# Performance work log

Hardware: AMD Instinct MI355X
Metric: run time of the kernel (lower is better)

## Reference

```python
import jax, jax.numpy as jnp
import numpy as np

BSZ, SL, K, D_IN, D_OUT = 2, 1024, 24, 512, 512
K_U, K_Y = 3, 2
USE_HANKEL_L = False


def get_top_eigh(l, k, use_hankel_L):
    i = np.arange(1, l + 1, dtype=np.float64)
    s = i[:, None] + i[None, :]
    if use_hankel_L:
        Z = ((-1.0) ** (s - 2.0) + 1.0) * 8.0 / ((s + 3.0) * (s - 1.0) * (s + 1.0))
    else:
        Z = 2.0 / (s ** 3 - s)
    sigma, phi = np.linalg.eigh(Z)  # ascending
    return jnp.asarray(sigma[-k:], jnp.float32), jnp.asarray(phi[:, -k:], jnp.float32)


def shift(x, k):
    # causal shift along time axis 1, zero-padded at the front
    if k == 0:
        return x
    return jnp.pad(x, ((0, 0), (k, 0), (0, 0)))[:, : x.shape[1]]


def fft_causal_conv(filters, u):
    # filters: (l, k); u: (b, l, d) -> (b, l, k, d) causal convolution per filter
    l = u.shape[1]
    n = 2 * l
    F = jnp.fft.rfft(filters, n=n, axis=0)  # (n//2+1, k)
    U = jnp.fft.rfft(u, n=n, axis=1)        # (b, n//2+1, d)
    Y = jnp.fft.irfft(U[:, :, None, :] * F[None, :, :, None], n=n, axis=1)
    return Y[:, :l].astype(u.dtype)


def compute_ar_u(M_u, u):
    # ar_u[b,t,o] = sum_{i<k_u} M_u[i] @ u_{t-i}
    U = jnp.stack([shift(u, i) for i in range(M_u.shape[0])])  # (k_u, b, l, d_in)
    return jnp.einsum('koi,kbli->blo', M_u, U)


def compute_spectral(u, sigma, phi, M_phi_plus, M_phi_minus, m_y):
    l = u.shape[1]
    phi_s = phi * sigma ** 0.25  # eigenvalue-scaled spectral filters (l, k)
    U_plus = fft_causal_conv(phi_s, u)  # (b, l, k, d_in)
    spec = jnp.einsum('blki,koi->blo', U_plus, M_phi_plus)
    if not USE_HANKEL_L:
        # negative-featurization branch: filters modulated by (-1)^i
        alt = ((-1.0) ** jnp.arange(l)).astype(u.dtype)
        U_minus = fft_causal_conv(phi_s * alt[:, None], u)
        spec = spec + jnp.einsum('blki,koi->blo', U_minus, M_phi_minus)
    if m_y is not None:
        spec = shift(spec, m_y.shape[0])  # spectral features enter at lag k_y (paper: t-2)
    return spec


def compute_ar_y(m_y, y):
    # true short linear recurrence on outputs:
    # yhat_t = y_t + sum_{i=1}^{k_y} m_y[i-1] @ yhat_{t-i}; returns the correction term
    k_y, d_out = m_y.shape[0], m_y.shape[1]
    b = y.shape[0]

    def step(carry, y_t):  # carry: (k_y, b, d_out) = [yhat_{t-1}, ..., yhat_{t-k_y}]
        ar_t = jnp.einsum('koj,kbj->bo', m_y, carry)
        yhat_t = y_t + ar_t
        carry = jnp.concatenate([yhat_t[None], carry[:-1]], axis=0)
        return carry, ar_t

    y_tl = jnp.swapaxes(y, 0, 1)  # (l, b, d_out)
    _, ar = jax.lax.scan(step, jnp.zeros((k_y, b, d_out), y.dtype), y_tl)
    return jnp.swapaxes(ar, 0, 1)


def setup_inputs() -> dict:
    key = jax.random.key(0)
    k0, k1, k2, k3, k4 = jax.random.split(key, 5)
    inputs = jax.random.normal(k0, (BSZ, SL, D_IN), jnp.float32)
    M_u = jax.random.normal(k1, (K_U, D_OUT, D_IN), jnp.float32) * 0.02
    M_phi_plus = jax.random.normal(k2, (K, D_OUT, D_IN), jnp.float32) * 0.02
    M_phi_minus = jax.random.normal(k3, (K, D_OUT, D_IN), jnp.float32) * 0.02
    m_y = jax.random.normal(k4, (K_Y, D_OUT, D_OUT), jnp.float32) * 0.02
    sigma, phi = get_top_eigh(SL, K, USE_HANKEL_L)
    return {'inputs': inputs, 'M_u': M_u, 'M_phi_plus': M_phi_plus,
            'M_phi_minus': M_phi_minus, 'm_y': m_y, 'sigma': sigma, 'phi': phi}


def reference(inputs, M_u, M_phi_plus, M_phi_minus, m_y, sigma, phi):
    ar_u = compute_ar_u(M_u, inputs)
    spectral = compute_spectral(inputs, sigma, phi, M_phi_plus, M_phi_minus, m_y)
    y_t = ar_u + spectral
    y_t = y_t + compute_ar_y(m_y, y_t)  # learnable_m_y=True branch
    return y_t  # dropout p=0.0 (identity)
```

## Files before the change

kernel.cpp:

```cpp
#include <hip/hip_runtime.h>
#include <hip/hip_bf16.h>


typedef unsigned short u16;
typedef __attribute__((ext_vector_type(8))) short  vshort8;
typedef __attribute__((ext_vector_type(4))) short  vshort4;
typedef __attribute__((ext_vector_type(4))) float  f32x4;
typedef __attribute__((ext_vector_type(4))) unsigned int vuint4;

__device__ __forceinline__ u16 f2b(float x) {
  __hip_bfloat16 h = __float2bfloat16(x);
  return __builtin_bit_cast(u16, h);
}
__device__ __forceinline__ float b2f(u16 x) {
  unsigned int u = ((unsigned int)x) << 16;
  return __builtin_bit_cast(float, u);
}

__device__ __forceinline__ void gll16(const u16* g, u16* l) {
  __builtin_amdgcn_global_load_lds((__attribute__((address_space(1))) void*)g,
                                   (__attribute__((address_space(3))) void*)l,
                                   16, 0, 0);
}

struct GB {
  const u16* A; const u16* B;
  float* Cf; u16* Cb;
  const float* zf; float* out;
  u16* A2T; u16* Au;
  const u16* zp;
  int M, N;
};

template<int V>
__global__ __launch_bounds__(256) void g2(GB a) {
  const int tid = threadIdx.x;
  int bn = blockIdx.x, bm = blockIdx.y;
  int zz = blockIdx.z;
  int cj = 0, cb = 0, cd = 0, slot = 0;
  int kbeg = 0, kend = 0;
  if (V == 0) {
    int f = blockIdx.x;
    int o = (f & 7) * 408 + (f >> 3);
    bm = o & 15; bn = o >> 4; kend = 512;
  }
  if (V == 1) {
    int f = blockIdx.x;
    int o = (f & 7) * 144 + (f >> 3);
    const int offs1[8] = {0, 256, 480, 672, 832, 960, 1056, 1120};
    cj = 0;
    if (o >= offs1[1]) cj = 1;
    if (o >= offs1[2]) cj = 2;
    if (o >= offs1[3]) cj = 3;
    if (o >= offs1[4]) cj = 4;
    if (o >= offs1[5]) cj = 5;
    if (o >= offs1[6]) cj = 6;
    if (o >= offs1[7]) cj = 7;
    int r = o - offs1[cj];
    int run = 8 - cj;
    int combo = r / run;
    bm = cj + (r - combo * run);
    int zzc = combo >> 2; bn = combo & 3;
    cb = zzc & 1; cd = bm - cj;
    slot = zzc * 8 + cj;
    kbeg = (zzc >> 1) * 1536; kend = kbeg + 1536;
  }
  if (V == 2) {
    int f = blockIdx.x;
    int o = (f & 7) * 68 + (f >> 3);
    const int offs2[16] = {0, 64, 124, 180, 232, 280, 324, 364,
                           400, 432, 460, 484, 504, 520, 532, 540};
    int s = 0;
#pragma unroll
    for (int c = 1; c < 16; ++c)
      if (o >= offs2[c]) s = c;
    int r = o - offs2[s];
    bm = s + (r >> 2); bn = r & 3;
    zz = s;
    kbeg = s * 1024; kend = kbeg + 1024;
  }
  const int m0 = bm * 128, n0 = bn * 128;
  if (V == 3 || V == 5 || V == 6 || V == 7) kend = 1024;

  __shared__ u16 smem[16384];
  f32x4 acc[4][4];
#pragma unroll
  for (int i = 0; i < 4; i++)
#pragma unroll
    for (int j = 0; j < 4; j++) acc[i][j] = f32x4{0.f, 0.f, 0.f, 0.f};

  const int lane = tid & 63, wv = tid >> 6, wr = wv >> 1, wc = wv & 1;
  const u16* Ap = a.A;
  if (V == 5) Ap = a.A + (size_t)zz * 524288;
  const u16* zpl = a.zp + lane * 8;

  auto gaddrA = [&](int it, int k0) -> const u16* {
    int lrow = (it * 4 + wv) * 16 + (lane & 15);
    int kk = k0 + ((lane >> 4) << 3);
    if (V == 0) return Ap + (size_t)(m0 + lrow) * 512 + kk;
    if (V == 1) return Ap + (size_t)cd * 786432 + (size_t)lrow * 6144 + kk;
    if (V == 2) {
      int m = m0 + lrow, j = m >> 6, b = (m >> 5) & 1, c = m & 31;
      int tau = kk >> 9, p = kk & 511;
      if (tau > j) return zpl;
      return Ap + (size_t)(b * 1024 + c * 32 + j - tau) * 512 + p;
    }
    if (V == 3) { int m = m0 + lrow; return (m < a.M) ? Ap + (size_t)m * 1024 + kk : zpl; }
    if (V == 5) return Ap + (size_t)(m0 + lrow) * 1024 + kk;
    if (V == 6) return (lrow < 64) ? Ap + (size_t)lrow * 1024 + kk : zpl;
    if (lrow < 32) {
      int b = lrow & 1, k2 = lrow >> 1;
      return Ap + (size_t)(b * 32 + 2 * k2) * 1024 + kk;
    }
    return zpl;
  };
  auto gaddrB = [&](int it, int k0) -> const u16* {
    int lrow = (it * 4 + wv) * 16 + (lane & 15);
    int kk = k0 + ((lane >> 4) << 3);
    int n = n0 + lrow;
    if (V == 0) return a.B + (size_t)n * 512 + kk;
    if (V == 1) {
      int kh = kk >> 7, sp = kk & 127;
      return a.B + (size_t)(cb * 512 + n) * 49152 + kh * 1024 + cj * 128 + sp;
    }
    if (V == 2) {
      int tau = kk >> 9, p = kk & 511;
      return a.B + (size_t)tau * 524288 + (size_t)n * 1024 + p;
    }
    if (V == 3) {
      int jn = n >> 9, o = n & 511;
      return a.B + (size_t)(jn + 1) * 524288 + (size_t)o * 1024 + kk;
    }
    if (V == 5) return a.B + (size_t)n * 1024 + kk;
    return (n < 512)
        ? a.B + (size_t)32 * 524288 + (size_t)n * 1024 + kk
        : a.B + (size_t)31 * 524288 + (size_t)(n - 512) * 1024 + kk;
  };

  auto stage = [&](int c, int k0) {
#pragma unroll
    for (int it = 0; it < 2; ++it) {
      int weff = wv + it * 4;
      gll16(gaddrA(it, k0), smem + c * 4096 + weff * 512);
      gll16(gaddrB(it, k0), smem + 8192 + c * 4096 + weff * 512);
    }
  };

  if (kbeg < kend) stage(0, kbeg);
  __syncthreads();
  int cur = 0;
  for (int k0 = kbeg; k0 < kend; k0 += 32) {
    if (k0 + 32 < kend) stage(cur ^ 1, k0 + 32);
    vshort8 af[4], bf_[4];
#pragma unroll
    for (int s = 0; s < 4; s++) {
      af[s]  = *(const vshort8*)&smem[cur * 4096 + (((wr * 4 + s) * 4 + (lane >> 4)) * 16 + (lane & 15)) * 8];
      bf_[s] = *(const vshort8*)&smem[8192 + cur * 4096 + (((wc * 4 + s) * 4 + (lane >> 4)) * 16 + (lane & 15)) * 8];
    }
#pragma unroll
    for (int i = 0; i < 4; i++)
#pragma unroll
      for (int j = 0; j < 4; j++)
        acc[i][j] = __builtin_amdgcn_mfma_f32_16x16x32_bf16(af[i], bf_[j], acc[i][j], 0, 0, 0);
    __syncthreads();
    cur ^= 1;
  }

  if (V == 0 && bn < 192) {
    const int strd = 136;
    const int b = m0 >> 10;
#pragma unroll
    for (int p = 0; p < 2; ++p) {
      __syncthreads();
#pragma unroll
      for (int i = 0; i < 4; i++) {
#pragma unroll
        for (int jl = 0; jl < 2; jl++) {
          int j = p * 2 + jl;
          f32x4 v = acc[i][j];
          int mloc = wr * 64 + i * 16 + ((lane >> 4) << 2);
          int phys = (lane & 15) + (jl << 4) + (wc << 5);
          vshort4 pk = { (short)f2b(v[0]), (short)f2b(v[1]),
                         (short)f2b(v[2]), (short)f2b(v[3]) };
          *(vshort4*)&smem[phys * strd + mloc] = pk;
        }
      }
      __syncthreads();
      int rowp = tid >> 2, t4 = tid & 3;
      int c15 = rowp & 15, jl = (rowp >> 4) & 1, wcp = rowp >> 5;
      int n = n0 + wcp * 64 + p * 32 + jl * 16 + c15;
      int o = n & 511, kh = n >> 9;
      int sbase = (m0 & 1023) + t4 * 32;
      u16* dst = a.A2T + (size_t)(b * 512 + o) * 49152 + (size_t)kh * 1024 + sbase;
      const u16* srcl = &smem[rowp * strd + t4 * 32];
#pragma unroll
      for (int q = 0; q < 4; ++q)
        *(vuint4*)(dst + q * 8) = *(const vuint4*)(srcl + q * 8);
    }
    return;
  }

#pragma unroll
  for (int i = 0; i < 4; i++) {
    int em = m0 + wr * 64 + i * 16 + ((lane >> 4) << 2);
#pragma unroll
    for (int j = 0; j < 4; j++) {
      int n = n0 + wc * 64 + j * 16 + (lane & 15);
      f32x4 v = acc[i][j];
      if (V == 0) {
        int b = em >> 10, s = em & 1023;
        int jj = (n - 24576) >> 9, o = n & 511;
#pragma unroll
        for (int t = 0; t < 4; t++)
          a.Au[((size_t)(b * 3 + jj) * 1024 + (s + t)) * 512 + o] = f2b(v[t]);
      } else if (V == 1) {
        u16* C = a.Cb + (size_t)slot * 524288;
#pragma unroll
        for (int t = 0; t < 4; t++) C[(size_t)(em + t) * 512 + n] = f2b(v[t]);
      } else if (V == 2) {
        float* C = a.Cf + (size_t)zz * 1048576;
#pragma unroll
        for (int t = 0; t < 4; t++) C[(size_t)(em + t) * 512 + n] = v[t];
      } else if (V == 3) {
        int jj = n >> 9, oo = n & 511;
#pragma unroll
        for (int t = 0; t < 4; t++) {
          int m = em + t;
          if (m < a.M) {
            int b = m >> 5, c = m & 31;
            float zv = a.zf[(size_t)(jj * 64 + b * 32 + c) * 512 + oo];
            a.out[(size_t)b * 524288 + (size_t)(c * 32 + jj) * 512 + oo] = v[t] + zv;
          }
        }
      } else if (V == 5) {
        u16* C = a.Cb + (size_t)zz * 524288;
#pragma unroll
        for (int t = 0; t < 4; t++) C[(size_t)(em + t) * 1024 + n] = f2b(v[t]);
      } else if (V == 6) {
        int jrow = (n < 512) ? 31 : 30, oo = n & 511;
#pragma unroll
        for (int t = 0; t < 4; t++) {
          int m = em + t;
          if (m < 62) {
            int b = m & 1, c = m >> 1;
            a.Cf[(size_t)m * 1024 + n] =
                v[t] + a.zf[(size_t)(jrow * 64 + b * 32 + (c + 1)) * 512 + oo];
          }
        }
      } else {
        int jrow = (n < 512) ? 31 : 30, oo = n & 511;
#pragma unroll
        for (int t = 0; t < 4; t++) {
          int m = em + t;
          if (m < 32) {
            int b = m & 1, k2 = m >> 1;
            float val = v[t] + a.zf[(size_t)(jrow * 64 + b * 32 + 2 * k2) * 512 + oo];
            a.Cb[(size_t)(b * 32 + 2 * k2 + 1) * 1024 + n] = f2b(val);
          }
        }
      }
    }
  }
}

__global__ void k_prep_X(const float* __restrict__ u, u16* __restrict__ X) {
  int i4 = (blockIdx.x * 256 + threadIdx.x) * 4;
  if (i4 >= 1048576) return;
  f32x4 v = *(const f32x4*)(u + i4);
  vshort4 pk = { (short)f2b(v[0]), (short)f2b(v[1]), (short)f2b(v[2]), (short)f2b(v[3]) };
  *(vshort4*)(X + i4) = pk;
}

__global__ void k_prep_phis(const float* __restrict__ phi, const float* __restrict__ sigma,
                            float* __restrict__ phis) {
  int i = blockIdx.x * 256 + threadIdx.x;
  if (i >= 1024 * 48) return;
  int tau = i / 48, kf = i % 48, k = (kf >= 24) ? kf - 24 : kf;
  float v = phi[tau * 24 + k] * powf(sigma[k], 0.25f);
  if (kf >= 24 && (tau & 1)) v = -v;
  phis[i] = v;
}

__global__ void k_prep_W1(const float* __restrict__ Mp, const float* __restrict__ Mm,
                          const float* __restrict__ Mu, u16* __restrict__ W1) {
  int i4 = (blockIdx.x * 256 + threadIdx.x) * 4;
  if (i4 >= 13369344) return;
  const float* src; int off;
  if (i4 < 6291456) { src = Mp; off = i4; }
  else if (i4 < 12582912) { src = Mm; off = i4 - 6291456; }
  else { src = Mu; off = i4 - 12582912; }
  f32x4 v = *(const f32x4*)(src + off);
  vshort4 pk = { (short)f2b(v[0]), (short)f2b(v[1]), (short)f2b(v[2]), (short)f2b(v[3]) };
  *(vshort4*)(W1 + i4) = pk;
}

__global__ void k_prep_Wtoep(const float* __restrict__ phis, u16* __restrict__ W) {
  int i = blockIdx.x * 256 + threadIdx.x;
  if (i >= 6291456) return;
  int kap = i % 6144, row = i / 6144;
  int tp = row & 127, d = row >> 7;
  int kh = kap >> 7, sp = kap & 127;
  int tau = d * 128 + tp - sp;
  W[i] = (tau >= 0 && tau < 1024) ? f2b(phis[tau * 48 + kh]) : (u16)0;
}

__global__ void k_initTop(const float* __restrict__ my, u16* __restrict__ Top) {
  int i = blockIdx.x * 256 + threadIdx.x;
  if (i >= 1048576) return;
  int mat = i >> 19, rem = i & 524287, o = rem >> 10, k = rem & 1023;
  u16 v;
  if (mat == 0) v = (k == o) ? (u16)0x3F80 : (u16)0;
  else v = (k < 512) ? f2b(my[o * 512 + k]) : f2b(my[262144 + o * 512 + (k - 512)]);
  Top[i] = v;
}

__global__ __launch_bounds__(256) void k_transT(const u16* __restrict__ Top,
                                                u16* __restrict__ STc, int c) {
  __shared__ u16 tile[64][72];
  int tx = blockIdx.x, ty = blockIdx.y;
  int tid = threadIdx.x;
  int r = tid >> 2, seg = tid & 3;
  int k = ty * 64 + r;
  const u16* src = (k < 512) ? Top + (size_t)c * 524288 + (size_t)k * 1024 + tx * 64
                             : Top + (size_t)(c - 1) * 524288 + (size_t)(k - 512) * 1024 + tx * 64;
  *(vuint4*)&tile[r][seg * 16]     = *(const vuint4*)(src + seg * 16);
  *(vuint4*)&tile[r][seg * 16 + 8] = *(const vuint4*)(src + seg * 16 + 8);
  __syncthreads();
  int n = tx * 64 + r;
  u16 tmp[16];
#pragma unroll
  for (int j = 0; j < 16; j++) tmp[j] = tile[seg * 16 + j][r];
  *(vuint4*)&STc[(size_t)n * 1024 + ty * 64 + seg * 16]     = *(vuint4*)&tmp[0];
  *(vuint4*)&STc[(size_t)n * 1024 + ty * 64 + seg * 16 + 8] = *(vuint4*)&tmp[8];
}

__device__ __forceinline__ void addp(float* acc, vuint4 v) {
  const unsigned int* vu = (const unsigned int*)&v;
#pragma unroll
  for (int e = 0; e < 4; ++e) {
    unsigned int pw = vu[e];
    acc[2 * e]     += __builtin_bit_cast(float, (pw & 0xffffu) << 16);
    acc[2 * e + 1] += __builtin_bit_cast(float, pw & 0xffff0000u);
  }
}

__global__ void k_combine(const u16* __restrict__ parts, const u16* __restrict__ Au,
                          u16* __restrict__ ybf) {
  int i = blockIdx.x * 256 + threadIdx.x;
  if (i >= 131072) return;
  int og = i & 63, t = (i >> 6) & 1023, b = i >> 16;
  float acc[8];
#pragma unroll
  for (int e = 0; e < 8; ++e) acc[e] = 0.f;
#pragma unroll
  for (int j = 0; j < 3; j++)
    if (t >= j)
      addp(acc, *(const vuint4*)(Au + ((size_t)(b * 3 + j) * 1024 + (t - j)) * 512 + og * 8));
  if (t >= 2) {
    int tp = t - 2, bmv = tp >> 7;
#pragma unroll
    for (int g = 0; g < 8; ++g) {
      if ((g & 1) != b) continue;
      const u16* base = parts + (size_t)(g * 8) * 524288 + (size_t)tp * 512 + og * 8;
      for (int j = 0; j <= bmv; ++j)
        addp(acc, *(const vuint4*)(base + (size_t)j * 524288));
    }
  }
  u16 o16[8];
#pragma unroll
  for (int e = 0; e < 8; ++e) o16[e] = f2b(acc[e]);
  *(vuint4*)(ybf + ((size_t)(b * 1024 + t)) * 512 + og * 8) = *(vuint4*)o16;
}

__global__ void k_zreduce(const float* __restrict__ zp, float* __restrict__ z) {
  int i = blockIdx.x * 256 + threadIdx.x;
  if (i >= 1048576) return;
  int nsum = (i >> 16) + 1;
  float s = 0.f;
  for (int j = 0; j < nsum; ++j) s += zp[(size_t)j * 1048576 + i];
  z[i] = s;
}

__global__ void k_wm(const float* __restrict__ zf, u16* __restrict__ Wm) {
  int i = blockIdx.x * 256 + threadIdx.x;
  if (i >= 65536) return;
  int row = i >> 10, n = i & 1023;
  int b = row & 1, c = row >> 1;
  int jrow = (n < 512) ? 31 : 30, oo = n & 511;
  Wm[i] = f2b(zf[(size_t)(jrow * 64 + b * 32 + c) * 512 + oo]);
}

__global__ __launch_bounds__(256) void k_bnd2(const u16* __restrict__ Top,
                                              const float* __restrict__ ubuf,
                                              float* __restrict__ bnd,
                                              u16* __restrict__ Abnd, int k) {
  __shared__ float st[2048];
  int tid = threadIdx.x;
  const float* s0 = bnd + (size_t)k * 2048;
  for (int j = tid; j < 2048; j += 256) st[j] = s0[j];
  __syncthreads();
  int q4 = blockIdx.x * 256 + tid;
  int q = q4 >> 2, quarter = q4 & 3;
  int b = q >> 10, kk = q & 1023;
  const u16* row = (kk < 512) ? Top + (size_t)64 * 524288 + (size_t)kk * 1024
                              : Top + (size_t)63 * 524288 + (size_t)(kk - 512) * 1024;
  const float* stb = st + b * 1024 + quarter * 256;
  const u16* rp = row + quarter * 256;
  float sum = 0.f;
  for (int t = 0; t < 32; ++t) {
    vuint4 v = *(const vuint4*)(rp + t * 8);
    const unsigned int* vu = (const unsigned int*)&v;
#pragma unroll
    for (int e = 0; e < 4; ++e) {
      unsigned int pw = vu[e];
      float lo = __builtin_bit_cast(float, (pw & 0xffffu) << 16);
      float hi = __builtin_bit_cast(float, pw & 0xffff0000u);
      sum += lo * stb[t * 8 + e * 2] + hi * stb[t * 8 + e * 2 + 1];
    }
  }
  sum += __shfl_xor(sum, 1);
  sum += __shfl_xor(sum, 2);
  if (quarter == 0) {
    float s = sum + ubuf[(size_t)(4 * k + b) * 1024 + kk];
    bnd[(size_t)(k + 1) * 2048 + b * 1024 + kk] = s;
    Abnd[(size_t)(b * 32 + 2 * k + 2) * 1024 + kk] = f2b(s);
  }
}

extern "C" void kernel_launch(void* const* d_in, const int* in_sizes, int n_in,
                              void* d_out, int out_size, void* d_ws, size_t ws_size,
                              hipStream_t stream) {
  const float* u     = (const float*)d_in[0];
  const float* Mu    = (const float*)d_in[1];
  const float* Mp    = (const float*)d_in[2];
  const float* Mm    = (const float*)d_in[3];
  const float* my    = (const float*)d_in[4];
  const float* sigma = (const float*)d_in[5];
  const float* phi   = (const float*)d_in[6];
  float* out = (float*)d_out;

  char* ws = (char*)d_ws;
  size_t off = 0;
  auto alc = [&](size_t b) { size_t p = off; off = (off + b + 255) & ~(size_t)255; return p; };
  u16*  X     = (u16*)(ws + alc(2097152));
  u16*  Wtoep = (u16*)(ws + alc(12582912));
  u16*  A2T   = (u16*)(ws + alc(100663296));
  u16*  Au    = (u16*)(ws + alc(6291456));
  u16*  W1    = (u16*)(ws + alc(26738688));
  char* ptail = ws + alc(40370176); (void)ptail;
  float* phis = (float*)(ws + alc(196608));
  float* bnd  = (float*)(ws + alc(131072));
  u16*  Abnd  = (u16*)(ws + alc(131072));
  u16*  Wm    = (u16*)(ws + alc(131072));
  float* ubuf = (float*)(ws + alc(262144));
  u16*  zpad  = (u16*)(ws + alc(32768));
  if (off > ws_size) return;
  u16*  partsBf = (u16*)W1;
  float* zparts = (float*)W1;
  u16*  ybf = A2T;
  float* zf = (float*)((char*)A2T + (4 << 20));
  u16*  Top = (u16*)((char*)A2T + (size_t)(8 << 20));
  u16*  STc = (u16*)((char*)A2T + (size_t)(76 << 20));

  hipMemsetAsync(zpad, 0, 32768, stream);

  k_prep_X<<<dim3(1024), 256, 0, stream>>>(u, X);
  k_prep_phis<<<dim3(192), 256, 0, stream>>>(phi, sigma, phis);
  k_prep_W1<<<dim3(13056), 256, 0, stream>>>(Mp, Mm, Mu, W1);
  k_prep_Wtoep<<<dim3(24576), 256, 0, stream>>>(phis, Wtoep);

  {
    GB g{}; g.A = X; g.B = W1; g.A2T = A2T; g.Au = Au; g.zp = zpad;
    g.M = 2048; g.N = 26112;
    g2<0><<<dim3(3264), 256, 0, stream>>>(g);
  }
  {
    GB g{}; g.A = Wtoep; g.B = A2T; g.Cb = partsBf; g.zp = zpad;
    g.M = 1024; g.N = 512;
    g2<1><<<dim3(1152), 256, 0, stream>>>(g);
  }
  k_combine<<<dim3(512), 256, 0, stream>>>(partsBf, Au, ybf);

  k_initTop<<<dim3(4096), 256, 0, stream>>>(my, Top);
  {
    const int cs[5] = {1, 2, 4, 8, 16};
    for (int li = 0; li < 5; ++li) {
      int c = cs[li];
      k_transT<<<dim3(16, 16), 256, 0, stream>>>(Top, STc, c);
      GB s{}; s.A = Top + 524288; s.B = STc; s.Cb = Top + (size_t)(c + 1) * 524288;
      s.zp = zpad; s.M = 512; s.N = 1024;
      g2<5><<<dim3(8, 4, c), 256, 0, stream>>>(s);
    }
    k_transT<<<dim3(16, 16), 256, 0, stream>>>(Top, STc, 32);
    GB s{}; s.A = Top + (size_t)31 * 524288; s.B = STc;
    s.Cb = Top + (size_t)63 * 524288; s.zp = zpad; s.M = 512; s.N = 1024;
    g2<5><<<dim3(8, 4, 2), 256, 0, stream>>>(s);
  }

  {
    GB g{}; g.A = ybf; g.B = Top; g.Cf = zparts; g.zp = zpad;
    g.M = 2048; g.N = 512;
    g2<2><<<dim3(544), 256, 0, stream>>>(g);
  }
  k_zreduce<<<dim3(4096), 256, 0, stream>>>(zparts, zf);

  k_wm<<<dim3(256), 256, 0, stream>>>(zf, Wm);
  {
    GB g{}; g.A = Wm; g.B = Top; g.Cf = ubuf; g.zf = zf; g.zp = zpad;
    g.M = 64; g.N = 1024;
    g2<6><<<dim3(8, 1, 1), 256, 0, stream>>>(g);
  }
  hipMemsetAsync(bnd, 0, 8192, stream);
  hipMemsetAsync(Abnd, 0, 131072, stream);
  for (int k = 0; k < 15; ++k)
    k_bnd2<<<dim3(32), 256, 0, stream>>>(Top, ubuf, bnd, Abnd, k);
  {
    GB g{}; g.A = Abnd; g.B = Top; g.Cb = Abnd; g.zf = zf; g.zp = zpad;
    g.M = 32; g.N = 1024;
    g2<7><<<dim3(8, 1, 1), 256, 0, stream>>>(g);
  }

  {
    GB g{}; g.A = Abnd; g.B = Top; g.zf = zf; g.out = out; g.zp = zpad;
    g.M = 64; g.N = 16384;
    g2<3><<<dim3(128, 1, 1), 256, 0, stream>>>(g);
  }
}
```

Before: 714.5 us.

## Widen projection GEMM tile to 128x256 with 512 threads, fuse prep and reduce kernels

The large input-projection GEMM (V0) now uses 128x256 tiles with 8 waves per block and half as many blocks. This lets each A tile feed more output columns and cuts redundant A loads. The transposed-store epilogue is rewritten so one wave column at a time writes through LDS. Separately, the X, W1 and Toeplitz prep kernels are merged into one launch, with the Toeplitz writes vectorised to 8 elements. The z-reduce, Wm build and the bnd/Abnd zeroing are folded into one kernel to cut launches and memsets. Risks: larger LDS use and 512-thread blocks may lower occupancy, and Abnd is now zeroed only partially.

```diff
diff --git a/kernel.cpp b/kernel.cpp
--- a/kernel.cpp
+++ b/kernel.cpp
@@ -33,7 +33,7 @@
 };
 
 template<int V>
-__global__ __launch_bounds__(256) void g2(GB a) {
+__global__ __launch_bounds__(V == 0 ? 512 : 256) void g2(GB a) {
   const int tid = threadIdx.x;
   int bn = blockIdx.x, bm = blockIdx.y;
   int zz = blockIdx.z;
@@ -41,7 +41,7 @@
   int kbeg = 0, kend = 0;
   if (V == 0) {
     int f = blockIdx.x;
-    int o = (f & 7) * 408 + (f >> 3);
+    int o = (f & 7) * 204 + (f >> 3);
     bm = o & 15; bn = o >> 4; kend = 512;
   }
   if (V == 1) {
@@ -79,17 +79,20 @@
     zz = s;
     kbeg = s * 1024; kend = kbeg + 1024;
   }
-  const int m0 = bm * 128, n0 = bn * 128;
+  const int m0 = bm * 128;
+  const int n0 = (V == 0) ? bn * 256 : bn * 128;
   if (V == 3 || V == 5 || V == 6 || V == 7) kend = 1024;
 
-  __shared__ u16 smem[16384];
+  __shared__ u16 smem[V == 0 ? 24576 : 16384];
   f32x4 acc[4][4];
 #pragma unroll
   for (int i = 0; i < 4; i++)
 #pragma unroll
     for (int j = 0; j < 4; j++) acc[i][j] = f32x4{0.f, 0.f, 0.f, 0.f};
 
-  const int lane = tid & 63, wv = tid >> 6, wr = wv >> 1, wc = wv & 1;
+  const int lane = tid & 63, wv = tid >> 6;
+  const int wr = (V == 0) ? (wv >> 2) : (wv >> 1);
+  const int wc = (V == 0) ? (wv & 3) : (wv & 1);
   const u16* Ap = a.A;
   if (V == 5) Ap = a.A + (size_t)zz * 524288;
   const u16* zpl = a.zp + lane * 8;
@@ -97,7 +100,6 @@
   auto gaddrA = [&](int it, int k0) -> const u16* {
     int lrow = (it * 4 + wv) * 16 + (lane & 15);
     int kk = k0 + ((lane >> 4) << 3);
-    if (V == 0) return Ap + (size_t)(m0 + lrow) * 512 + kk;
     if (V == 1) return Ap + (size_t)cd * 786432 + (size_t)lrow * 6144 + kk;
     if (V == 2) {
       int m = m0 + lrow, j = m >> 6, b = (m >> 5) & 1, c = m & 31;
@@ -118,7 +120,6 @@
     int lrow = (it * 4 + wv) * 16 + (lane & 15);
     int kk = k0 + ((lane >> 4) << 3);
     int n = n0 + lrow;
-    if (V == 0) return a.B + (size_t)n * 512 + kk;
     if (V == 1) {
       int kh = kk >> 7, sp = kk & 127;
       return a.B + (size_t)(cb * 512 + n) * 49152 + kh * 1024 + cj * 128 + sp;
@@ -138,11 +139,23 @@
   };
 
   auto stage = [&](int c, int k0) {
-#pragma unroll
-    for (int it = 0; it < 2; ++it) {
-      int weff = wv + it * 4;
-      gll16(gaddrA(it, k0), smem + c * 4096 + weff * 512);
-      gll16(gaddrB(it, k0), smem + 8192 + c * 4096 + weff * 512);
+    if (V == 0) {
+      int kk = k0 + ((lane >> 4) << 3);
+      int lrowA = wv * 16 + (lane & 15);
+      gll16(Ap + (size_t)(m0 + lrowA) * 512 + kk, smem + c * 4096 + wv * 512);
+#pragma unroll
+      for (int it = 0; it < 2; ++it) {
+        int lrowB = (it * 8 + wv) * 16 + (lane & 15);
+        gll16(a.B + (size_t)(n0 + lrowB) * 512 + kk,
+              smem + 8192 + c * 8192 + (it * 8 + wv) * 512);
+      }
+    } else {
+#pragma unroll
+      for (int it = 0; it < 2; ++it) {
+        int weff = wv + it * 4;
+        gll16(gaddrA(it, k0), smem + c * 4096 + weff * 512);
+        gll16(gaddrB(it, k0), smem + 8192 + c * 4096 + weff * 512);
+      }
     }
   };
 
@@ -154,8 +167,14 @@
     vshort8 af[4], bf_[4];
 #pragma unroll
     for (int s = 0; s < 4; s++) {
-      af[s]  = *(const vshort8*)&smem[cur * 4096 + (((wr * 4 + s) * 4 + (lane >> 4)) * 16 + (lane & 15)) * 8];
-      bf_[s] = *(const vshort8*)&smem[8192 + cur * 4096 + (((wc * 4 + s) * 4 + (lane >> 4)) * 16 + (lane & 15)) * 8];
+      af[s] = *(const vshort8*)&smem[cur * 4096 +
+                (((wr * 4 + s) * 4 + (lane >> 4)) * 16 + (lane & 15)) * 8];
+      if (V == 0)
+        bf_[s] = *(const vshort8*)&smem[8192 + cur * 8192 +
+                  (((wc * 4 + s) * 4 + (lane >> 4)) * 16 + (lane & 15)) * 8];
+      else
+        bf_[s] = *(const vshort8*)&smem[8192 + cur * 4096 +
+                  (((wc * 4 + s) * 4 + (lane >> 4)) * 16 + (lane & 15)) * 8];
     }
 #pragma unroll
     for (int i = 0; i < 4; i++)
@@ -166,36 +185,35 @@
     cur ^= 1;
   }
 
-  if (V == 0 && bn < 192) {
+  if (V == 0 && bn < 96) {
     const int strd = 136;
     const int b = m0 >> 10;
 #pragma unroll
-    for (int p = 0; p < 2; ++p) {
+    for (int p = 0; p < 4; ++p) {
       __syncthreads();
-#pragma unroll
-      for (int i = 0; i < 4; i++) {
-#pragma unroll
-        for (int jl = 0; jl < 2; jl++) {
-          int j = p * 2 + jl;
-          f32x4 v = acc[i][j];
-          int mloc = wr * 64 + i * 16 + ((lane >> 4) << 2);
-          int phys = (lane & 15) + (jl << 4) + (wc << 5);
-          vshort4 pk = { (short)f2b(v[0]), (short)f2b(v[1]),
-                         (short)f2b(v[2]), (short)f2b(v[3]) };
-          *(vshort4*)&smem[phys * strd + mloc] = pk;
+      if (wc == p) {
+#pragma unroll
+        for (int i = 0; i < 4; i++) {
+#pragma unroll
+          for (int j = 0; j < 4; j++) {
+            f32x4 v = acc[i][j];
+            int mloc = wr * 64 + i * 16 + ((lane >> 4) << 2);
+            int phys = j * 16 + (lane & 15);
+            vshort4 pk = { (short)f2b(v[0]), (short)f2b(v[1]),
+                           (short)f2b(v[2]), (short)f2b(v[3]) };
+            *(vshort4*)&smem[phys * strd + mloc] = pk;
+          }
         }
       }
       __syncthreads();
-      int rowp = tid >> 2, t4 = tid & 3;
-      int c15 = rowp & 15, jl = (rowp >> 4) & 1, wcp = rowp >> 5;
-      int n = n0 + wcp * 64 + p * 32 + jl * 16 + c15;
+      int rowp = tid >> 3, t8 = tid & 7;
+      int n = n0 + p * 64 + rowp;
       int o = n & 511, kh = n >> 9;
-      int sbase = (m0 & 1023) + t4 * 32;
+      int sbase = (m0 & 1023) + t8 * 16;
       u16* dst = a.A2T + (size_t)(b * 512 + o) * 49152 + (size_t)kh * 1024 + sbase;
-      const u16* srcl = &smem[rowp * strd + t4 * 32];
-#pragma unroll
-      for (int q = 0; q < 4; ++q)
-        *(vuint4*)(dst + q * 8) = *(const vuint4*)(srcl + q * 8);
+      const u16* srcl = &smem[rowp * strd + t8 * 16];
+      *(vuint4*)(dst)     = *(const vuint4*)(srcl);
+      *(vuint4*)(dst + 8) = *(const vuint4*)(srcl + 8);
     }
     return;
   }
@@ -263,14 +281,6 @@
   }
 }
 
-__global__ void k_prep_X(const float* __restrict__ u, u16* __restrict__ X) {
-  int i4 = (blockIdx.x * 256 + threadIdx.x) * 4;
-  if (i4 >= 1048576) return;
-  f32x4 v = *(const f32x4*)(u + i4);
-  vshort4 pk = { (short)f2b(v[0]), (short)f2b(v[1]), (short)f2b(v[2]), (short)f2b(v[3]) };
-  *(vshort4*)(X + i4) = pk;
-}
-
 __global__ void k_prep_phis(const float* __restrict__ phi, const float* __restrict__ sigma,
                             float* __restrict__ phis) {
   int i = blockIdx.x * 256 + threadIdx.x;
@@ -281,27 +291,46 @@
   phis[i] = v;
 }
 
-__global__ void k_prep_W1(const float* __restrict__ Mp, const float* __restrict__ Mm,
-                          const float* __restrict__ Mu, u16* __restrict__ W1) {
-  int i4 = (blockIdx.x * 256 + threadIdx.x) * 4;
-  if (i4 >= 13369344) return;
-  const float* src; int off;
-  if (i4 < 6291456) { src = Mp; off = i4; }
-  else if (i4 < 12582912) { src = Mm; off = i4 - 6291456; }
-  else { src = Mu; off = i4 - 12582912; }
-  f32x4 v = *(const f32x4*)(src + off);
-  vshort4 pk = { (short)f2b(v[0]), (short)f2b(v[1]), (short)f2b(v[2]), (short)f2b(v[3]) };
-  *(vshort4*)(W1 + i4) = pk;
-}
-
-__global__ void k_prep_Wtoep(const float* __restrict__ phis, u16* __restrict__ W) {
-  int i = blockIdx.x * 256 + threadIdx.x;
-  if (i >= 6291456) return;
-  int kap = i % 6144, row = i / 6144;
-  int tp = row & 127, d = row >> 7;
-  int kh = kap >> 7, sp = kap & 127;
-  int tau = d * 128 + tp - sp;
-  W[i] = (tau >= 0 && tau < 1024) ? f2b(phis[tau * 48 + kh]) : (u16)0;
+__global__ void k_prep_all(const float* __restrict__ u, const float* __restrict__ Mp,
+                           const float* __restrict__ Mm, const float* __restrict__ Mu,
+                           const float* __restrict__ phis,
+                           u16* __restrict__ X, u16* __restrict__ W1,
+                           u16* __restrict__ Wtoep) {
+  int gid = blockIdx.x * 256 + threadIdx.x;
+  if (gid < 262144) {
+    int i4 = gid * 4;
+    f32x4 v = *(const f32x4*)(u + i4);
+    vshort4 pk = { (short)f2b(v[0]), (short)f2b(v[1]), (short)f2b(v[2]), (short)f2b(v[3]) };
+    *(vshort4*)(X + i4) = pk;
+  }
+#pragma unroll
+  for (int r = 0; r < 4; ++r) {
+    int item = gid + r * 1048576;
+    if (item < 3342336) {
+      int i4 = item * 4;
+      const float* src; int off;
+      if (i4 < 6291456) { src = Mp; off = i4; }
+      else if (i4 < 12582912) { src = Mm; off = i4 - 6291456; }
+      else { src = Mu; off = i4 - 12582912; }
+      f32x4 v = *(const f32x4*)(src + off);
+      vshort4 pk = { (short)f2b(v[0]), (short)f2b(v[1]), (short)f2b(v[2]), (short)f2b(v[3]) };
+      *(vshort4*)(W1 + i4) = pk;
+    }
+  }
+  if (gid < 786432) {
+    int i = gid * 8;
+    int kap = i % 6144, row = i / 6144;
+    int tp = row & 127, d = row >> 7;
+    int kh = kap >> 7, sp = kap & 127;
+    int tau0 = d * 128 + tp - sp;
+    u16 vals[8];
+#pragma unroll
+    for (int e = 0; e < 8; ++e) {
+      int tau = tau0 - e;
+      vals[e] = (tau >= 0 && tau < 1024) ? f2b(phis[tau * 48 + kh]) : (u16)0;
+    }
+    *(vuint4*)(Wtoep + i) = *(const vuint4*)vals;
+  }
 }
 
 __global__ void k_initTop(const float* __restrict__ my, u16* __restrict__ Top) {
@@ -372,22 +401,20 @@
   *(vuint4*)(ybf + ((size_t)(b * 1024 + t)) * 512 + og * 8) = *(vuint4*)o16;
 }
 
-__global__ void k_zreduce(const float* __restrict__ zp, float* __restrict__ z) {
+__global__ void k_zred(const float* __restrict__ zp, float* __restrict__ z,
+                       u16* __restrict__ Wm, float* __restrict__ bnd,
+                       u16* __restrict__ Abnd) {
   int i = blockIdx.x * 256 + threadIdx.x;
+  if (i < 2048) bnd[i] = 0.f;
+  if (i < 1024) { Abnd[i] = 0; Abnd[32768 + i] = 0; }
   if (i >= 1048576) return;
   int nsum = (i >> 16) + 1;
   float s = 0.f;
   for (int j = 0; j < nsum; ++j) s += zp[(size_t)j * 1048576 + i];
   z[i] = s;
-}
-
-__global__ void k_wm(const float* __restrict__ zf, u16* __restrict__ Wm) {
-  int i = blockIdx.x * 256 + threadIdx.x;
-  if (i >= 65536) return;
-  int row = i >> 10, n = i & 1023;
-  int b = row & 1, c = row >> 1;
-  int jrow = (n < 512) ? 31 : 30, oo = n & 511;
-  Wm[i] = f2b(zf[(size_t)(jrow * 64 + b * 32 + c) * 512 + oo]);
+  int m = i >> 9, jj = m >> 6, rem = m & 63, b = rem >> 5, c = rem & 31, oo = i & 511;
+  if (jj == 31) Wm[(size_t)((c << 1) | b) * 1024 + oo] = f2b(s);
+  if (jj == 30) Wm[(size_t)((c << 1) | b) * 1024 + 512 + oo] = f2b(s);
 }
 
 __global__ __launch_bounds__(256) void k_bnd2(const u16* __restrict__ Top,
@@ -464,15 +491,13 @@
 
   hipMemsetAsync(zpad, 0, 32768, stream);
 
-  k_prep_X<<<dim3(1024), 256, 0, stream>>>(u, X);
   k_prep_phis<<<dim3(192), 256, 0, stream>>>(phi, sigma, phis);
-  k_prep_W1<<<dim3(13056), 256, 0, stream>>>(Mp, Mm, Mu, W1);
-  k_prep_Wtoep<<<dim3(24576), 256, 0, stream>>>(phis, Wtoep);
+  k_prep_all<<<dim3(4096), 256, 0, stream>>>(u, Mp, Mm, Mu, phis, X, W1, Wtoep);
 
   {
     GB g{}; g.A = X; g.B = W1; g.A2T = A2T; g.Au = Au; g.zp = zpad;
     g.M = 2048; g.N = 26112;
-    g2<0><<<dim3(3264), 256, 0, stream>>>(g);
+    g2<0><<<dim3(1632), 512, 0, stream>>>(g);
   }
   {
     GB g{}; g.A = Wtoep; g.B = A2T; g.Cb = partsBf; g.zp = zpad;
@@ -502,16 +527,13 @@
     g.M = 2048; g.N = 512;
     g2<2><<<dim3(544), 256, 0, stream>>>(g);
   }
-  k_zreduce<<<dim3(4096), 256, 0, stream>>>(zparts, zf);
-
-  k_wm<<<dim3(256), 256, 0, stream>>>(zf, Wm);
+  k_zred<<<dim3(4096), 256, 0, stream>>>(zparts, zf, Wm, bnd, Abnd);
+
   {
     GB g{}; g.A = Wm; g.B = Top; g.Cf = ubuf; g.zf = zf; g.zp = zpad;
     g.M = 64; g.N = 1024;
     g2<6><<<dim3(8, 1, 1), 256, 0, stream>>>(g);
   }
-  hipMemsetAsync(bnd, 0, 8192, stream);
-  hipMemsetAsync(Abnd, 0, 131072, stream);
   for (int k = 0; k < 15; ++k)
     k_bnd2<<<dim3(32), 256, 0, stream>>>(Top, ubuf, bnd, Abnd, k);
   {
```

Result: no change. 702.6 us (-1.7%).
